# Kernel optimization log

Measured on AMD Instinct MI355X. Metric: run time of the kernel, lower is better.

Reference implementation:

```python
import jax, jax.numpy as jnp
import numpy as np

IN_CH, OUT_CH, K, STRIDE, PAD, NUM_POINTS = 16, 32, 3, 1, 1, 3
NUM_INPUTS = IN_CH * K * K  # 144
BATCH, H, W = 8, 32, 32


def setup_inputs() -> dict:
    key = jax.random.key(0)
    k1, k2, k3 = jax.random.split(key, 3)
    x = jax.random.normal(k1, (BATCH, IN_CH, H, W), dtype=jnp.float32)
    # sorted breakpoint positions per (input, output) pair in [-1, 1]
    base = jnp.linspace(-1.0, 1.0, NUM_POINTS, dtype=jnp.float32)
    jitter = 0.2 * (jax.random.uniform(k2, (NUM_INPUTS, OUT_CH, NUM_POINTS), dtype=jnp.float32) - 0.5) / NUM_POINTS
    positions = jnp.sort(base[None, None, :] + jitter, axis=-1)  # (I, O, P), sorted
    values = 0.1 * jax.random.normal(k3, (NUM_INPUTS, OUT_CH, NUM_POINTS), dtype=jnp.float32)
    return {"x": x, "positions": positions, "values": values}


def _gather_pt(table, idx):
    # table: (I, O, P), idx: (N, I, O) -> (N, I, O)
    return jnp.take_along_axis(table[None], idx[..., None], axis=-1)[..., 0]


def _piecewise(patches, positions, values):
    # patches: (N, I); positions/values: (I, O, P)
    P = positions.shape[-1]
    # bucket index: number of breakpoints <= x, clipped to a valid segment
    cmp = patches[:, :, None, None] >= positions[None]       # (N, I, O, P)
    idx = jnp.clip(cmp.sum(axis=-1) - 1, 0, P - 2)           # (N, I, O)
    pl = _gather_pt(positions, idx)
    pr = _gather_pt(positions, idx + 1)
    vl = _gather_pt(values, idx)
    vr = _gather_pt(values, idx + 1)
    t = (patches[:, :, None] - pl) / (pr - pl)               # (N, I, O)
    y = vl + t * (vr - vl)                                   # per-pair piecewise-linear value
    return y.sum(axis=1)                                     # (N, O): sum over input dims


def reference(x, positions, values):
    B, C, Hi, Wi = x.shape
    Ho = (Hi + 2 * PAD - K) // STRIDE + 1
    Wo = (Wi + 2 * PAD - K) // STRIDE + 1
    # im2col / unfold: (B, C*K*K, Ho, Wo) with (c, kh, kw) feature ordering like torch unfold
    patches = jax.lax.conv_general_dilated_patches(
        x, (K, K), (STRIDE, STRIDE), ((PAD, PAD), (PAD, PAD)))
    patches = patches.reshape(B, NUM_INPUTS, Ho * Wo).transpose(0, 2, 1).reshape(-1, NUM_INPUTS)
    out = _piecewise(patches, positions, values)             # (B*Ho*Wo, O)
    out = out.reshape(B, Ho * Wo, OUT_CH).transpose(0, 2, 1)
    return out.reshape(B, OUT_CH, Ho, Wo)
```

## Files before the change

kernel.cpp:

```cpp
#include <hip/hip_runtime.h>

#define IN_CH 16
#define OUT_CH 32
#define NUM_INPUTS 144
#define H_ 32
#define W_ 32
#define TILE_H 4
#define LDS_H 6
#define LDS_W 34
#define CHW (LDS_H * LDS_W)

typedef __attribute__((ext_vector_type(2))) float f32x2;

__global__ __launch_bounds__(256, 2) void apc_fused(
        const float* __restrict__ x,
        const float* __restrict__ pos,
        const float* __restrict__ val,
        float* __restrict__ out) {
    __shared__ float  lx[IN_CH * CHW];
    __shared__ float4 ltPM[2 * NUM_INPUTS];
    __shared__ f32x2  ltD [2 * NUM_INPUTS];
    __shared__ f32x2  ltB [2 * NUM_INPUTS];
    __shared__ float4 lred[128];

    int bx  = blockIdx.x;
    int b   = bx >> 3;
    int ho0 = (bx & 7) * TILE_H;
    int g   = blockIdx.y;
    int tid = threadIdx.x;

    for (int idx = tid; idx < IN_CH * CHW; idx += 256) {
        int c   = idx / CHW;
        int rem = idx - c * CHW;
        int r   = rem / LDS_W;
        int col = rem - r * LDS_W;
        int gr  = ho0 + r - 1;
        int gc  = col - 1;
        float v = 0.f;
        if ((unsigned)gr < (unsigned)H_ && (unsigned)gc < (unsigned)W_)
            v = x[((b * IN_CH + c) * H_ + gr) * W_ + gc];
        lx[idx] = v;
    }

    if (tid < NUM_INPUTS) {
        const float4* pp = (const float4*)(pos + tid * 96 + g * 12);
        const float4* vv = (const float4*)(val + tid * 96 + g * 12);
        float4 pA = pp[0], pB = pp[1], pC = pp[2];
        float4 vA = vv[0], vB = vv[1], vC = vv[2];
        float P[12] = {pA.x,pA.y,pA.z,pA.w, pB.x,pB.y,pB.z,pB.w, pC.x,pC.y,pC.z,pC.w};
        float V[12] = {vA.x,vA.y,vA.z,vA.w, vB.x,vB.y,vB.z,vB.w, vC.x,vC.y,vC.z,vC.w};
        float p1[4], m0[4], dm[4], b0[4];
        #pragma unroll
        for (int k = 0; k < 4; ++k) {
            float q0 = P[3*k], q1 = P[3*k+1], q2 = P[3*k+2];
            float w0 = V[3*k], w1 = V[3*k+1], w2 = V[3*k+2];
            float s0 = (w1 - w0) / (q1 - q0);
            float s1 = (w2 - w1) / (q2 - q1);
            p1[k] = q1; m0[k] = s0; dm[k] = s1 - s0; b0[k] = w0 - s0 * q0;
        }
        ltPM[tid]              = make_float4(p1[0], p1[1], m0[0], m0[1]);
        ltD [tid]              = (f32x2){dm[0], dm[1]};
        ltB [tid]              = (f32x2){b0[0], b0[1]};
        ltPM[NUM_INPUTS + tid] = make_float4(p1[2], p1[3], m0[2], m0[3]);
        ltD [NUM_INPUTS + tid] = (f32x2){dm[2], dm[3]};
        ltB [NUM_INPUTS + tid] = (f32x2){b0[2], b0[3]};
    }
    __syncthreads();

    int col  = tid & 31;
    int trow = (tid >> 5) & 1;
    int pgrp = (tid >> 6) & 1;
    int cs   = tid >> 7;
    int i0   = cs * 72;
    int tb0  = pgrp * NUM_INPUTS + i0;
    int base = (2 * trow) * LDS_W + col;
    int lane = tid & 63;

    f32x2 bb = ltB[tb0 + lane];
    if (lane < 8) bb += ltB[tb0 + 64 + lane];
    #pragma unroll
    for (int m = 1; m < 64; m <<= 1) {
        bb.x += __shfl_xor(bb.x, m);
        bb.y += __shfl_xor(bb.y, m);
    }

    f32x2 aA = {0,0}, hA = {0,0};
    f32x2 aB = {0,0}, hB = {0,0};
    const f32x2 zz = {0.f, 0.f};

    #pragma unroll
    for (int cc = 0; cc < 8; ++cc) {
        int c = cs * 8 + cc;
        #pragma unroll
        for (int kw = 0; kw < 3; ++kw) {
            float p0 = lx[c * CHW + base + 0 * LDS_W + kw];
            float p1 = lx[c * CHW + base + 1 * LDS_W + kw];
            float p2 = lx[c * CHW + base + 2 * LDS_W + kw];
            float p3 = lx[c * CHW + base + 3 * LDS_W + kw];
            float pa[4] = {p0, p1, p2, p3};
            #pragma unroll
            for (int kh = 0; kh < 3; ++kh) {
                int ti = pgrp * NUM_INPUTS + (c * 3 + kh) * 3 + kw;
                float4 q = ltPM[ti];
                f32x2  D = ltD[ti];
                f32x2  P = {q.x, q.y}, M = {q.z, q.w};
                f32x2 qA = {pa[kh],     pa[kh]};
                f32x2 qB = {pa[kh + 1], pa[kh + 1]};
                aA = __builtin_elementwise_fma(M, qA, aA);
                hA = __builtin_elementwise_fma(D, __builtin_elementwise_max(qA - P, zz), hA);
                aB = __builtin_elementwise_fma(M, qB, aB);
                hB = __builtin_elementwise_fma(D, __builtin_elementwise_max(qB - P, zz), hB);
            }
        }
    }

    f32x2 rA = aA + hA + bb;
    f32x2 rB = aB + hB + bb;

    if (cs == 1)
        lred[tid - 128] = make_float4(rA.x, rA.y, rB.x, rB.y);
    __syncthreads();
    if (cs == 0) {
        float4 q = lred[tid];
        rA.x += q.x; rA.y += q.y; rB.x += q.z; rB.y += q.w;
        int hoA = ho0 + 2 * trow;
        int o0  = 4 * g + 2 * pgrp;
        int HW  = H_ * W_;
        int ob  = ((b * OUT_CH + o0) * H_ + hoA) * W_ + col;
        out[ob          ] = rA.x;
        out[ob +      HW] = rA.y;
        out[ob + W_     ] = rB.x;
        out[ob + W_ + HW] = rB.y;
    }
}

extern "C" void kernel_launch(void* const* d_in, const int* in_sizes, int n_in,
                              void* d_out, int out_size, void* d_ws, size_t ws_size,
                              hipStream_t stream) {
    const float* x   = (const float*)d_in[0];
    const float* pos = (const float*)d_in[1];
    const float* val = (const float*)d_in[2];

    dim3 grid(64, 8);
    apc_fused<<<grid, 256, 0, stream>>>(x, pos, val, (float*)d_out);
}
```

Baseline: 66.52 us.

## Retile kernel to 2x8 spatial tiles covering all outputs per block

Each block now handles a 2x8 output pixel tile for all 32 output channels. Previously a block handled a 4-row strip for 4 outputs. The 512 threads are split so that each wave owns two input channels and each lane covers 2 outputs by 4 pixels. Partial sums are reduced across waves through LDS, and the bias term is folded into the table build. The table build uses the fast reciprocal and is spread across all threads. This changes the x-halo reuse and table-load balance, but every block now rebuilds the full 144x32 table, which adds redundant work across 512 blocks.

```diff
diff --git a/kernel.cpp b/kernel.cpp
--- a/kernel.cpp
+++ b/kernel.cpp
@@ -5,132 +5,149 @@
 #define NUM_INPUTS 144
 #define H_ 32
 #define W_ 32
-#define TILE_H 4
-#define LDS_H 6
-#define LDS_W 34
-#define CHW (LDS_H * LDS_W)
 
 typedef __attribute__((ext_vector_type(2))) float f32x2;
+typedef __attribute__((ext_vector_type(4))) float f32x4;
 
-__global__ __launch_bounds__(256, 2) void apc_fused(
+__global__ __launch_bounds__(512, 4) void apc_fused(
         const float* __restrict__ x,
         const float* __restrict__ pos,
         const float* __restrict__ val,
         float* __restrict__ out) {
-    __shared__ float  lx[IN_CH * CHW];
-    __shared__ float4 ltPM[2 * NUM_INPUTS];
-    __shared__ f32x2  ltD [2 * NUM_INPUTS];
-    __shared__ f32x2  ltB [2 * NUM_INPUTS];
-    __shared__ float4 lred[128];
+    __shared__ f32x4 ltA[NUM_INPUTS * 16];
+    __shared__ f32x2 ltD[NUM_INPUTS * 16];
+    __shared__ float lx[IN_CH * 4 * 16];
+    __shared__ f32x2 bpart[512];
+    __shared__ f32x2 B0f[16];
 
-    int bx  = blockIdx.x;
-    int b   = bx >> 3;
-    int ho0 = (bx & 7) * TILE_H;
-    int g   = blockIdx.y;
-    int tid = threadIdx.x;
+    int tid  = threadIdx.x;
+    int bx   = blockIdx.x;
+    int b    = bx >> 6;
+    int t64  = bx & 63;
+    int row0 = (t64 >> 2) * 2;
+    int col0 = (t64 & 3) * 8;
 
-    for (int idx = tid; idx < IN_CH * CHW; idx += 256) {
-        int c   = idx / CHW;
-        int rem = idx - c * CHW;
-        int r   = rem / LDS_W;
-        int col = rem - r * LDS_W;
-        int gr  = ho0 + r - 1;
-        int gc  = col - 1;
+    #pragma unroll
+    for (int it = 0; it < 2; ++it) {
+        int s  = tid + it * 512;
+        int c  = s >> 6;
+        int rr = (s >> 4) & 3;
+        int cl = s & 15;
+        int gr = row0 + rr - 1;
+        int gc = col0 + cl - 1;
         float v = 0.f;
-        if ((unsigned)gr < (unsigned)H_ && (unsigned)gc < (unsigned)W_)
+        if (cl < 10 && (unsigned)gr < (unsigned)H_ && (unsigned)gc < (unsigned)W_)
             v = x[((b * IN_CH + c) * H_ + gr) * W_ + gc];
-        lx[idx] = v;
+        lx[s] = v;
     }
 
-    if (tid < NUM_INPUTS) {
-        const float4* pp = (const float4*)(pos + tid * 96 + g * 12);
-        const float4* vv = (const float4*)(val + tid * 96 + g * 12);
-        float4 pA = pp[0], pB = pp[1], pC = pp[2];
-        float4 vA = vv[0], vB = vv[1], vC = vv[2];
-        float P[12] = {pA.x,pA.y,pA.z,pA.w, pB.x,pB.y,pB.z,pB.w, pC.x,pC.y,pC.z,pC.w};
-        float V[12] = {vA.x,vA.y,vA.z,vA.w, vB.x,vB.y,vB.z,vB.w, vC.x,vC.y,vC.z,vC.w};
-        float p1[4], m0[4], dm[4], b0[4];
+    {
+        int opb = tid & 15;
+        int ib  = tid >> 4;
+        f32x2 bs = {0.f, 0.f};
         #pragma unroll
-        for (int k = 0; k < 4; ++k) {
-            float q0 = P[3*k], q1 = P[3*k+1], q2 = P[3*k+2];
-            float w0 = V[3*k], w1 = V[3*k+1], w2 = V[3*k+2];
-            float s0 = (w1 - w0) / (q1 - q0);
-            float s1 = (w2 - w1) / (q2 - q1);
-            p1[k] = q1; m0[k] = s0; dm[k] = s1 - s0; b0[k] = w0 - s0 * q0;
+        for (int k = 0; k < 5; ++k) {
+            int i = ib + 32 * k;
+            if (i < NUM_INPUTS) {
+                const float* pp = pos + i * 96 + opb * 6;
+                const float* vv = val + i * 96 + opb * 6;
+                float q0a = pp[0], q1a = pp[1], q2a = pp[2];
+                float q0b = pp[3], q1b = pp[4], q2b = pp[5];
+                float w0a = vv[0], w1a = vv[1], w2a = vv[2];
+                float w0b = vv[3], w1b = vv[4], w2b = vv[5];
+                float s0a = (w1a - w0a) * __builtin_amdgcn_rcpf(q1a - q0a);
+                float s1a = (w2a - w1a) * __builtin_amdgcn_rcpf(q2a - q1a);
+                float s0b = (w1b - w0b) * __builtin_amdgcn_rcpf(q1b - q0b);
+                float s1b = (w2b - w1b) * __builtin_amdgcn_rcpf(q2b - q1b);
+                ltA[i * 16 + opb] = (f32x4){q1a, q1b, s0a, s0b};
+                ltD[i * 16 + opb] = (f32x2){s1a - s0a, s1b - s0b};
+                bs.x += w0a - s0a * q0a;
+                bs.y += w0b - s0b * q0b;
+            }
         }
-        ltPM[tid]              = make_float4(p1[0], p1[1], m0[0], m0[1]);
-        ltD [tid]              = (f32x2){dm[0], dm[1]};
-        ltB [tid]              = (f32x2){b0[0], b0[1]};
-        ltPM[NUM_INPUTS + tid] = make_float4(p1[2], p1[3], m0[2], m0[3]);
-        ltD [NUM_INPUTS + tid] = (f32x2){dm[2], dm[3]};
-        ltB [NUM_INPUTS + tid] = (f32x2){b0[2], b0[3]};
+        bpart[tid] = bs;
     }
     __syncthreads();
 
-    int col  = tid & 31;
-    int trow = (tid >> 5) & 1;
-    int pgrp = (tid >> 6) & 1;
-    int cs   = tid >> 7;
-    int i0   = cs * 72;
-    int tb0  = pgrp * NUM_INPUTS + i0;
-    int base = (2 * trow) * LDS_W + col;
-    int lane = tid & 63;
-
-    f32x2 bb = ltB[tb0 + lane];
-    if (lane < 8) bb += ltB[tb0 + 64 + lane];
-    #pragma unroll
-    for (int m = 1; m < 64; m <<= 1) {
-        bb.x += __shfl_xor(bb.x, m);
-        bb.y += __shfl_xor(bb.y, m);
+    if (tid < 16) {
+        f32x2 s = {0.f, 0.f};
+        #pragma unroll
+        for (int g2 = 0; g2 < 32; ++g2) s += bpart[g2 * 16 + tid];
+        B0f[tid] = s;
     }
 
-    f32x2 aA = {0,0}, hA = {0,0};
-    f32x2 aB = {0,0}, hB = {0,0};
+    int wid  = tid >> 6;
+    int lane = tid & 63;
+    int sg   = lane >> 4;
+    int op   = lane & 15;
+    int r0   = sg >> 1;
+    int cb   = (sg & 1) * 4;
+    int c0   = wid * 2;
+
+    f32x2 aacc[4], hacc[4];
     const f32x2 zz = {0.f, 0.f};
+    #pragma unroll
+    for (int j = 0; j < 4; ++j) { aacc[j] = zz; hacc[j] = zz; }
+
+    const float* lxb = lx + (c0 * 4 + r0) * 16 + cb;
+    const f32x4* Ab  = ltA + c0 * 144 + op;
+    const f32x2* Db  = ltD + c0 * 144 + op;
 
     #pragma unroll
-    for (int cc = 0; cc < 8; ++cc) {
-        int c = cs * 8 + cc;
+    for (int dc = 0; dc < 2; ++dc) {
+        float w[3][6];
         #pragma unroll
-        for (int kw = 0; kw < 3; ++kw) {
-            float p0 = lx[c * CHW + base + 0 * LDS_W + kw];
-            float p1 = lx[c * CHW + base + 1 * LDS_W + kw];
-            float p2 = lx[c * CHW + base + 2 * LDS_W + kw];
-            float p3 = lx[c * CHW + base + 3 * LDS_W + kw];
-            float pa[4] = {p0, p1, p2, p3};
+        for (int dr = 0; dr < 3; ++dr) {
+            f32x4 u = *(const f32x4*)(lxb + (dc * 4 + dr) * 16);
+            f32x2 v = *(const f32x2*)(lxb + (dc * 4 + dr) * 16 + 4);
+            w[dr][0] = u.x; w[dr][1] = u.y; w[dr][2] = u.z; w[dr][3] = u.w;
+            w[dr][4] = v.x; w[dr][5] = v.y;
+        }
+        #pragma unroll
+        for (int kh = 0; kh < 3; ++kh) {
             #pragma unroll
-            for (int kh = 0; kh < 3; ++kh) {
-                int ti = pgrp * NUM_INPUTS + (c * 3 + kh) * 3 + kw;
-                float4 q = ltPM[ti];
-                f32x2  D = ltD[ti];
-                f32x2  P = {q.x, q.y}, M = {q.z, q.w};
-                f32x2 qA = {pa[kh],     pa[kh]};
-                f32x2 qB = {pa[kh + 1], pa[kh + 1]};
-                aA = __builtin_elementwise_fma(M, qA, aA);
-                hA = __builtin_elementwise_fma(D, __builtin_elementwise_max(qA - P, zz), hA);
-                aB = __builtin_elementwise_fma(M, qB, aB);
-                hB = __builtin_elementwise_fma(D, __builtin_elementwise_max(qB - P, zz), hB);
+            for (int kw = 0; kw < 3; ++kw) {
+                int ti = (dc * 9 + kh * 3 + kw) * 16;
+                f32x4 A = Ab[ti];
+                f32x2 D = Db[ti];
+                f32x2 P = {A.x, A.y};
+                f32x2 M = {A.z, A.w};
+                #pragma unroll
+                for (int j = 0; j < 4; ++j) {
+                    f32x2 q = {w[kh][kw + j], w[kh][kw + j]};
+                    aacc[j] = __builtin_elementwise_fma(M, q, aacc[j]);
+                    hacc[j] = __builtin_elementwise_fma(
+                        D, __builtin_elementwise_max(q - P, zz), hacc[j]);
+                }
             }
         }
     }
 
-    f32x2 rA = aA + hA + bb;
-    f32x2 rB = aB + hB + bb;
+    __syncthreads();
+    {
+        f32x2 s0 = aacc[0] + hacc[0], s1 = aacc[1] + hacc[1];
+        f32x2 s2 = aacc[2] + hacc[2], s3 = aacc[3] + hacc[3];
+        int rb = (wid * 64 + lane) * 2;
+        ltA[rb + 0] = (f32x4){s0.x, s0.y, s1.x, s1.y};
+        ltA[rb + 1] = (f32x4){s2.x, s2.y, s3.x, s3.y};
+    }
+    __syncthreads();
 
-    if (cs == 1)
-        lred[tid - 128] = make_float4(rA.x, rA.y, rB.x, rB.y);
-    __syncthreads();
-    if (cs == 0) {
-        float4 q = lred[tid];
-        rA.x += q.x; rA.y += q.y; rB.x += q.z; rB.y += q.w;
-        int hoA = ho0 + 2 * trow;
-        int o0  = 4 * g + 2 * pgrp;
-        int HW  = H_ * W_;
-        int ob  = ((b * OUT_CH + o0) * H_ + hoA) * W_ + col;
-        out[ob          ] = rA.x;
-        out[ob +      HW] = rA.y;
-        out[ob + W_     ] = rB.x;
-        out[ob + W_ + HW] = rB.y;
+    if (tid < 256) {
+        const f32x2* red = (const f32x2*)ltA;
+        int opx = tid >> 4;
+        int p   = tid & 15;
+        int rr  = p >> 3;
+        int cl  = p & 7;
+        int sgx = rr * 2 + (cl >> 2);
+        int j   = cl & 3;
+        int base = (sgx * 16 + opx) * 4 + j;
+        f32x2 s = B0f[opx];
+        #pragma unroll
+        for (int wv = 0; wv < 8; ++wv) s += red[wv * 256 + base];
+        int oidx = ((b * OUT_CH + 2 * opx) * H_ + (row0 + rr)) * W_ + (col0 + cl);
+        out[oidx]            = s.x;
+        out[oidx + H_ * W_]  = s.y;
     }
 }
 
@@ -141,6 +158,5 @@
     const float* pos = (const float*)d_in[1];
     const float* val = (const float*)d_in[2];
 
-    dim3 grid(64, 8);
-    apc_fused<<<grid, 256, 0, stream>>>(x, pos, val, (float*)d_out);
+    apc_fused<<<dim3(512), dim3(512), 0, stream>>>(x, pos, val, (float*)d_out);
 }
```

After: 63.74 us. -4.2%, faster.
